# Optimization experiments

Measured on AMD Instinct MI355X. Metric: run time of the kernel, lower is better.

Reference implementation:

```python
import jax, jax.numpy as jnp
import numpy as np

NL, D, H, DK, L, F, P, NC, PS = 2, 128, 8, 16, 197, 256, 8, 1000, 16
EPS = 1e-5


def _ln(x, w, b):
    m = jnp.mean(x, -1, keepdims=True)
    v = jnp.mean((x - m) ** 2, -1, keepdims=True)
    return (x - m) * jax.lax.rsqrt(v + EPS) * w + b


def _trop_lin(x, W, b):
    # max-plus (tropical) linear: y_o = max_i (x_i + W[o, i]) + b_o
    return jnp.max(x[..., None, :] + W, axis=-1) + b


def _forward(x, patch_w, patch_b, cls_token, pos_embed, bn_gamma, bn_beta, bn_run_max, bn_run_range,
             n1_w, n1_b, n2_w, n2_b, wq, bq, wk, bk, wv, bv, wo, bo, gate_w, gate_b, temp,
             tu_w, tu_b, lf_a, lf_c, lf_gate, cu_w, cu_b, fg_w, fg_b, dn_w, dn_b,
             fn_w, fn_b, head_w, head_b):
    B, C, Hh, Ww = x.shape
    p = PS
    # patchify: [B,C,H,W] -> [B,num_patches,C*p*p]
    xp = x.reshape(B, C, Hh // p, p, Ww // p, p).transpose(0, 2, 4, 1, 3, 5).reshape(B, -1, C * p * p)
    h = xp @ patch_w.T + patch_b
    h = jnp.concatenate([jnp.broadcast_to(cls_token, (B, 1, D)), h], axis=1) + pos_embed
    # TropicalBatchNorm (eval mode, running buffers)
    h = bn_gamma * ((h - bn_run_max) / (bn_run_range + EPS)) + bn_beta
    scale = DK ** -0.5
    for i in range(NL):
        hn = _ln(h, n1_w[i], n1_b[i])
        Q = _trop_lin(hn, wq[i], bq[i]).reshape(B, L, H, DK).transpose(0, 2, 1, 3)
        K = _trop_lin(hn, wk[i], bk[i]).reshape(B, L, H, DK).transpose(0, 2, 1, 3)
        V = (hn @ wv[i].T + bv[i]).reshape(B, L, H, DK).transpose(0, 2, 1, 3)
        cs = jnp.einsum('bhqd,bhkd->bhqk', Q, K) * scale
        # tropical max-plus scores: max_d(Q_q + K_k)  -> [B,H,L,L]
        ts = jnp.max(Q[:, :, :, None, :] + K[:, :, None, :, :], axis=-1) * scale
        g = jax.nn.sigmoid(hn @ gate_w[i].T + gate_b[i]).transpose(0, 2, 1)[..., None]  # [B,H,L,1]
        attn = jax.nn.softmax((g * ts + (1.0 - g) * cs) / temp[i][None, :, None, None], axis=-1)
        out = jnp.einsum('bhqk,bhkd->bhqd', attn, V).transpose(0, 2, 1, 3).reshape(B, L, D)
        h = h + (out @ wo[i].T + bo[i])
        hn2 = _ln(h, n2_w[i], n2_b[i])
        z = _trop_lin(hn2, tu_w[i], tu_b[i])                 # [B,L,F]
        zp = z[:, :, None, :] * lf_a[i] + lf_c[i]            # [B,L,P,F]
        gl = jax.nn.sigmoid(lf_gate[i])
        trop = gl * jnp.max(zp, axis=2) + (1.0 - gl) * jnp.min(zp, axis=2)
        classical = jax.nn.gelu(hn2 @ cu_w[i].T + cu_b[i], approximate=False)
        gf = jax.nn.sigmoid(hn2 @ fg_w[i].T + fg_b[i])
        fused = gf * trop + (1.0 - gf) * classical
        h = h + (fused @ dn_w[i].T + dn_b[i])
    h = _ln(h, fn_w, fn_b)
    return h[:, 0] @ head_w.T + head_b


def setup_inputs() -> dict:
    ks = iter(jax.random.split(jax.random.key(0), 64))
    rn = lambda shape, s=0.02: jax.random.normal(next(ks), shape, jnp.float32) * s
    return dict(
        x=jax.random.normal(next(ks), (4, 3, 224, 224), jnp.float32),
        patch_w=rn((D, 3 * PS * PS)), patch_b=jnp.zeros((D,), jnp.float32),
        cls_token=rn((1, 1, D)), pos_embed=rn((1, L, D)),
        bn_gamma=jnp.ones((D,), jnp.float32), bn_beta=jnp.zeros((D,), jnp.float32),
        bn_run_max=jnp.zeros((D,), jnp.float32), bn_run_range=jnp.ones((D,), jnp.float32),
        n1_w=jnp.ones((NL, D), jnp.float32) + rn((NL, D)), n1_b=rn((NL, D)),
        n2_w=jnp.ones((NL, D), jnp.float32) + rn((NL, D)), n2_b=rn((NL, D)),
        wq=rn((NL, D, D)), bq=rn((NL, D)),
        wk=rn((NL, D, D)), bk=rn((NL, D)),
        wv=rn((NL, D, D)), bv=rn((NL, D)),
        wo=rn((NL, D, D)), bo=rn((NL, D)),
        gate_w=rn((NL, H, D)), gate_b=2.0 + rn((NL, H)),
        temp=1.0 + 0.1 * jax.random.uniform(next(ks), (NL, H), jnp.float32),
        tu_w=rn((NL, F, D)), tu_b=rn((NL, F)),
        lf_a=rn((NL, P, F), 0.5), lf_c=rn((NL, P, F), 0.1), lf_gate=rn((NL, F), 0.5),
        cu_w=rn((NL, F, D)), cu_b=rn((NL, F)),
        fg_w=rn((NL, F, D)), fg_b=2.0 + rn((NL, F)),
        dn_w=rn((NL, D, F)), dn_b=rn((NL, D)),
        fn_w=jnp.ones((D,), jnp.float32) + rn((D,)), fn_b=rn((D,)),
        head_w=rn((NC, D)), head_b=jnp.zeros((NC,), jnp.float32),
    )


def reference(x, patch_w, patch_b, cls_token, pos_embed, bn_gamma, bn_beta, bn_run_max, bn_run_range,
              n1_w, n1_b, n2_w, n2_b, wq, bq, wk, bk, wv, bv, wo, bo, gate_w, gate_b, temp,
              tu_w, tu_b, lf_a, lf_c, lf_gate, cu_w, cu_b, fg_w, fg_b, dn_w, dn_b,
              fn_w, fn_b, head_w, head_b):
    return _forward(x, patch_w, patch_b, cls_token, pos_embed, bn_gamma, bn_beta, bn_run_max, bn_run_range,
                    n1_w, n1_b, n2_w, n2_b, wq, bq, wk, bk, wv, bv, wo, bo, gate_w, gate_b, temp,
                    tu_w, tu_b, lf_a, lf_c, lf_gate, cu_w, cu_b, fg_w, fg_b, dn_w, dn_b,
                    fn_w, fn_b, head_w, head_b)
```

## Files before the change

### kernel.cpp

```cpp
#include <hip/hip_runtime.h>
#include <math.h>

#define EPSF 1e-5f

__device__ __forceinline__ float sigm(float v){ return 1.f/(1.f+__expf(-v)); }

#define WS_H    0
#define WS_Q    100864
#define WS_K    201728
#define WS_V    302592
#define WS_G    403456
#define WS_AO   409760
#define WS_PWT  510624
#define WS_WQT  608928
#define WS_WKT  641696
#define WS_WVT  674464
#define WS_WOT  707232
#define WS_GWT  740000
#define WS_TUT  742048
#define WS_CUT  807584
#define WS_FGT  873120
#define WS_DNT  938656
#define WS_HDT  1004192

__global__ __launch_bounds__(256) void k_tr(
    const float* __restrict__ pw, const float* __restrict__ wq, const float* __restrict__ wk,
    const float* __restrict__ wv, const float* __restrict__ wo, const float* __restrict__ gw,
    const float* __restrict__ tu, const float* __restrict__ cu, const float* __restrict__ fg,
    const float* __restrict__ dn, const float* __restrict__ hd, float* __restrict__ ws)
{
    __shared__ float tile[32][33];
    int tn = blockIdx.x, t = threadIdx.x;

    if (tn >= 608) {
        for (int i=t;i<2048;i+=256){
            int m=i>>10, rem=i&1023, k=rem>>3, hh=rem&7;
            ws[WS_GWT + m*1024 + k*8 + hh] = gw[m*1024 + hh*128 + k];
        }
        return;
    }

    const float* srcp; long dstoff; int N, K, NR, nt, kt;
    if (tn < 96) {
        srcp=pw; dstoff=WS_PWT; N=128; K=768; NR=128; nt=tn/24; kt=tn%24;
    } else if (tn < 224) {
        int i2=tn-96, inst=i2>>4, lt=i2&15, m2=inst>>1;
        srcp = (m2==0)?wq:(m2==1)?wk:(m2==2)?wv:wo;
        srcp += (inst&1)*16384;
        dstoff = WS_WQT + (long)m2*32768 + (inst&1)*16384;
        N=128; K=128; NR=128; nt=lt>>2; kt=lt&3;
    } else if (tn < 416) {
        int i2=tn-224, inst=i2>>5, lt=i2&31, m2=inst>>1;
        srcp = (m2==0)?tu:(m2==1)?cu:fg;
        srcp += (inst&1)*32768;
        dstoff = WS_TUT + (long)m2*65536 + (inst&1)*32768;
        N=256; K=128; NR=256; nt=lt>>2; kt=lt&3;
    } else if (tn < 480) {
        int i2=tn-416, inst=i2>>5, lt=i2&31;
        srcp = dn + inst*32768; dstoff = WS_DNT + (long)inst*32768;
        N=128; K=256; NR=128; nt=lt>>3; kt=lt&7;
    } else {
        int lt=tn-480; srcp=hd; dstoff=WS_HDT; N=1000; K=128; NR=1000; nt=lt>>2; kt=lt&3;
    }

    int n0=nt*32, k0=kt*32;
    int tr=t>>3, tc=(t&7)*4;
    float4 v={0.f,0.f,0.f,0.f};
    if (n0+tr < NR) v = *(const float4*)(srcp + (size_t)(n0+tr)*K + k0 + tc);
    tile[tr][tc]=v.x; tile[tr][tc+1]=v.y; tile[tr][tc+2]=v.z; tile[tr][tc+3]=v.w;
    __syncthreads();
    int kr=t>>3, nc=(t&7)*4;
    float o0=tile[nc][kr], o1=tile[nc+1][kr], o2=tile[nc+2][kr], o3=tile[nc+3][kr];
    float* dp = ws + dstoff + (size_t)(k0+kr)*N + n0 + nc;
    if (n0+nc+3 < NR) {
        float4 o4={o0,o1,o2,o3};
        *(float4*)dp = o4;
    } else {
        if (n0+nc   < NR) dp[0]=o0;
        if (n0+nc+1 < NR) dp[1]=o1;
        if (n0+nc+2 < NR) dp[2]=o2;
        if (n0+nc+3 < NR) dp[3]=o3;
    }
}

__device__ __forceinline__ void ln512(float hv,
    const float* __restrict__ lw, const float* __restrict__ lb,
    float* hnS, float* red, int t)
{
    int r = t >> 7, d = t & 127;
    float s = hv, s2 = hv*hv;
    #pragma unroll
    for (int o=1;o<64;o<<=1){ s += __shfl_xor(s,o); s2 += __shfl_xor(s2,o); }
    int wid = t >> 6;
    if ((t & 63) == 0){ red[wid] = s; red[8+wid] = s2; }
    __syncthreads();
    float S  = red[2*r]   + red[2*r+1];
    float S2 = red[8+2*r] + red[8+2*r+1];
    float mu = S*(1.f/128.f), var = S2*(1.f/128.f)-mu*mu;
    float rr = rsqrtf(var+EPSF);
    hnS[r*128+d] = (hv-mu)*rr*lw[d]+lb[d];
    __syncthreads();
}

__device__ __forceinline__ void qkvT512(const float* hnS, float* pacc, int r0, int t,
    const float* __restrict__ wqT, const float* __restrict__ bq,
    const float* __restrict__ wkT, const float* __restrict__ bk,
    const float* __restrict__ wvT, const float* __restrict__ bv,
    const float* __restrict__ gwT, const float* __restrict__ gb,
    float* __restrict__ Q, float* __restrict__ Kg, float* __restrict__ V,
    float* __restrict__ g)
{
    if (t < 384) {
        int mat = t >> 7, q4i = t & 31, ks = (t >> 5) & 3;
        const float* wT = (mat==0) ? wqT : (mat==1) ? wkT : wvT;
        const float4* w4 = (const float4*)wT + q4i;
        float4 acc[4];
        if (mat < 2) {
            #pragma unroll
            for (int r=0;r<4;++r){ acc[r].x=acc[r].y=acc[r].z=acc[r].w=-1e30f; }
            #pragma unroll
            for (int kb=0;kb<2;++kb){
                float4 wv16[16];
                #pragma unroll
                for (int j=0;j<16;++j) wv16[j]=w4[(ks*32+kb*16+j)*32];
                #pragma unroll
                for (int j=0;j<16;++j){
                    float4 w=wv16[j];
                    #pragma unroll
                    for (int r=0;r<4;++r){
                        float av = hnS[r*128 + ks*32+kb*16+j];
                        acc[r].x=fmaxf(acc[r].x,av+w.x); acc[r].y=fmaxf(acc[r].y,av+w.y);
                        acc[r].z=fmaxf(acc[r].z,av+w.z); acc[r].w=fmaxf(acc[r].w,av+w.w);
                    }
                }
            }
        } else {
            #pragma unroll
            for (int r=0;r<4;++r){ acc[r].x=acc[r].y=acc[r].z=acc[r].w=0.f; }
            #pragma unroll
            for (int kb=0;kb<2;++kb){
                float4 wv16[16];
                #pragma unroll
                for (int j=0;j<16;++j) wv16[j]=w4[(ks*32+kb*16+j)*32];
                #pragma unroll
                for (int j=0;j<16;++j){
                    float4 w=wv16[j];
                    #pragma unroll
                    for (int r=0;r<4;++r){
                        float av = hnS[r*128 + ks*32+kb*16+j];
                        acc[r].x=fmaf(av,w.x,acc[r].x); acc[r].y=fmaf(av,w.y,acc[r].y);
                        acc[r].z=fmaf(av,w.z,acc[r].z); acc[r].w=fmaf(av,w.w,acc[r].w);
                    }
                }
            }
        }
        #pragma unroll
        for (int r=0;r<4;++r)
            *(float4*)(pacc + mat*2048 + ks*512 + r*128 + q4i*4) = acc[r];
    } else {
        int u = t & 127, r = u>>5, hh=(u>>2)&7, ks=u&3;
        const float* a = hnS + r*128;
        float acc = 0.f;
        #pragma unroll
        for (int kb=0;kb<2;++kb){
            float wv16[16];
            #pragma unroll
            for (int j=0;j<16;++j) wv16[j]=gwT[(ks*32+kb*16+j)*8+hh];
            #pragma unroll
            for (int j=0;j<16;++j) acc = fmaf(a[ks*32+kb*16+j], wv16[j], acc);
        }
        acc += __shfl_xor(acc,1);
        acc += __shfl_xor(acc,2);
        if (ks==0) g[(r0+r)*8+hh] = sigm(acc + gb[hh]);
    }
    __syncthreads();
    if (t < 384) {
        int mat=t>>7, d=t&127;
        float* dst = (mat==0) ? Q : (mat==1) ? Kg : V;
        const float* bias = (mat==0) ? bq : (mat==1) ? bk : bv;
        #pragma unroll
        for (int r=0;r<4;++r){
            float p0 = pacc[mat*2048 + 0*512 + r*128 + d];
            float p1 = pacc[mat*2048 + 1*512 + r*128 + d];
            float p2 = pacc[mat*2048 + 2*512 + r*128 + d];
            float p3 = pacc[mat*2048 + 3*512 + r*128 + d];
            float s = (mat < 2) ? fmaxf(fmaxf(p0,p1), fmaxf(p2,p3))
                                : (p0 + p1 + p2 + p3);
            dst[(size_t)(r0+r)*128 + d] = s + bias[d];
        }
    }
}

__global__ __launch_bounds__(512) void k_p1(
    const float* __restrict__ x, const float* __restrict__ pwT, const float* __restrict__ pb,
    const float* __restrict__ clsT, const float* __restrict__ pos,
    const float* __restrict__ bng, const float* __restrict__ bnb,
    const float* __restrict__ bnm, const float* __restrict__ bnr,
    const float* __restrict__ n1w, const float* __restrict__ n1b,
    const float* __restrict__ wqT, const float* __restrict__ bq,
    const float* __restrict__ wkT, const float* __restrict__ bk,
    const float* __restrict__ wvT, const float* __restrict__ bv,
    const float* __restrict__ gwT, const float* __restrict__ gb,
    float* __restrict__ h, float* __restrict__ Q, float* __restrict__ Kg,
    float* __restrict__ V, float* __restrict__ g)
{
    __shared__ __align__(16) float xp[4*768];
    __shared__ __align__(16) float pacc[8192];
    __shared__ __align__(16) float hnS[512];
    __shared__ float red[16];
    int t = threadIdx.x, r0 = blockIdx.x * 4;

    #pragma unroll
    for (int r=0;r<4;++r){
        int row=r0+r, b=row/197, l=row-b*197;
        if (l>0){
            int patch=l-1, ph=patch/14, pc=patch-ph*14;
            const float* xb = x + (size_t)b*150528 + ph*3584 + pc*16;
            for (int i=t;i<768;i+=512){
                int c=i>>8, rr=(i>>4)&15, cc=i&15;
                xp[r*768+i] = xb[c*50176 + rr*224 + cc];
            }
        }
    }
    __syncthreads();

    {
        int q4i = t & 31, ks = t >> 5;
        float4 acc[4];
        #pragma unroll
        for (int r=0;r<4;++r){ acc[r].x=acc[r].y=acc[r].z=acc[r].w=0.f; }
        const float4* w4 = (const float4*)pwT + q4i;
        #pragma unroll
        for (int kb=0;kb<3;++kb){
            float4 wv16[16];
            #pragma unroll
            for (int j=0;j<16;++j) wv16[j]=w4[(ks*48+kb*16+j)*32];
            #pragma unroll
            for (int j=0;j<16;++j){
                float4 w=wv16[j];
                #pragma unroll
                for (int r=0;r<4;++r){
                    float av = xp[r*768 + ks*48+kb*16+j];
                    acc[r].x=fmaf(av,w.x,acc[r].x); acc[r].y=fmaf(av,w.y,acc[r].y);
                    acc[r].z=fmaf(av,w.z,acc[r].z); acc[r].w=fmaf(av,w.w,acc[r].w);
                }
            }
        }
        #pragma unroll
        for (int r=0;r<4;++r)
            *(float4*)(pacc + (ks*4+r)*128 + q4i*4) = acc[r];
    }
    __syncthreads();

    float hres;
    {
        int r=t>>7, d=t&127;
        int row=r0+r, l=row%197;
        float s = 0.f;
        #pragma unroll
        for (int ks=0;ks<16;++ks) s += pacc[(ks*4+r)*128+d];
        float v = (l==0) ? clsT[d] : (s + pb[d]);
        v += pos[l*128+d];
        v = bng[d]*((v-bnm[d])/(bnr[d]+EPSF))+bnb[d];
        hres=v;
        h[row*128+d]=v;
    }
    __syncthreads();
    ln512(hres, n1w, n1b, hnS, red, t);
    qkvT512(hnS, pacc, r0, t, wqT,bq,wkT,bk,wvT,bv,gwT,gb, Q,Kg,V,g);
}

__global__ __launch_bounds__(256) void k_attn(
    const float* __restrict__ Qd, const float* __restrict__ Kd,
    const float* __restrict__ Vd, const float* __restrict__ gd,
    const float* __restrict__ tempL, float* __restrict__ ao)
{
    __shared__ __align__(16) float Ks[197*20];
    __shared__ __align__(16) float Vs[197*20];
    int bid = blockIdx.x, t = threadIdx.x;
    int qc = bid % 7, bh = bid / 7, hh = bh & 7, b = bh >> 3;
    size_t base = (size_t)(b*197)*128 + hh*16;

    {
        const float4* ksrc=(const float4*)(Kd+base);
        const float4* vsrc=(const float4*)(Vd+base);
        float4* kdst=(float4*)Ks; float4* vdst=(float4*)Vs;
        for (int idx=t; idx<788; idx+=256){
            int l=idx>>2, jj=idx&3;
            kdst[l*5+jj]=ksrc[l*32+jj];
            vdst[l*5+jj]=vsrc[l*32+jj];
        }
    }
    __syncthreads();

    int q = qc*32 + (t>>3), j8 = t&7;
    if (q >= 197) return;

    float Qr[16];
    {
        const float4* qp=(const float4*)(Qd+base+(size_t)q*128);
        #pragma unroll
        for (int u=0;u<4;++u){
            float4 v=qp[u];
            Qr[4*u]=v.x; Qr[4*u+1]=v.y; Qr[4*u+2]=v.z; Qr[4*u+3]=v.w;
        }
    }
    float gq = gd[(b*197+q)*8+hh];
    float it = 0.25f / tempL[hh];
    float gg = gq*it, cg = (1.f-gq)*it;

    float m=-1e30f, lsum=0.f, o[16];
    #pragma unroll
    for (int j=0;j<16;++j) o[j]=0.f;

    for (int k=j8;k<197;k+=8){
        const float4* kr4=(const float4*)(Ks+k*20);
        float4 kv0=kr4[0], kv1=kr4[1], kv2=kr4[2], kv3=kr4[3];
        float kr[16] = {kv0.x,kv0.y,kv0.z,kv0.w, kv1.x,kv1.y,kv1.z,kv1.w,
                        kv2.x,kv2.y,kv2.z,kv2.w, kv3.x,kv3.y,kv3.z,kv3.w};
        float cs=0.f, ts=-1e30f;
        #pragma unroll
        for (int j=0;j<16;++j){
            cs=fmaf(Qr[j],kr[j],cs);
            ts=fmaxf(ts,Qr[j]+kr[j]);
        }
        float sc=fmaf(gg,ts,cg*cs);
        if (sc>m){
            float c=__expf(m-sc);
            lsum*=c;
            #pragma unroll
            for (int j=0;j<16;++j) o[j]*=c;
            m=sc;
        }
        float p=__expf(sc-m);
        lsum+=p;
        const float4* vr4=(const float4*)(Vs+k*20);
        float4 vv0=vr4[0], vv1=vr4[1], vv2=vr4[2], vv3=vr4[3];
        float vr[16] = {vv0.x,vv0.y,vv0.z,vv0.w, vv1.x,vv1.y,vv1.z,vv1.w,
                        vv2.x,vv2.y,vv2.z,vv2.w, vv3.x,vv3.y,vv3.z,vv3.w};
        #pragma unroll
        for (int j=0;j<16;++j) o[j]=fmaf(p,vr[j],o[j]);
    }

    #pragma unroll
    for (int mask=1;mask<8;mask<<=1){
        float mo=__shfl_xor(m,mask), lo=__shfl_xor(lsum,mask);
        float mn=fmaxf(m,mo);
        float ea=__expf(m-mn), eb=__expf(mo-mn);
        lsum=lsum*ea+lo*eb;
        #pragma unroll
        for (int j=0;j<16;++j){
            float oo=__shfl_xor(o[j],mask);
            o[j]=o[j]*ea+oo*eb;
        }
        m=mn;
    }

    if (j8==0){
        float inv=1.f/lsum;
        float* orow=ao+base+(size_t)q*128;
        #pragma unroll
        for (int j=0;j<16;++j) orow[j]=o[j]*inv;
    }
}

template <int FINAL>
__global__ __launch_bounds__(512) void k_p34(
    const float* __restrict__ ao, float* __restrict__ h,
    const float* __restrict__ woT, const float* __restrict__ bo,
    const float* __restrict__ n2w, const float* __restrict__ n2b,
    const float* __restrict__ tuT, const float* __restrict__ tub,
    const float* __restrict__ laA, const float* __restrict__ laC,
    const float* __restrict__ lgG,
    const float* __restrict__ cuT, const float* __restrict__ cub,
    const float* __restrict__ fgT, const float* __restrict__ fgb,
    const float* __restrict__ dnT, const float* __restrict__ dnb,
    const float* __restrict__ nlw, const float* __restrict__ nlb,
    const float* __restrict__ wqT, const float* __restrict__ bq,
    const float* __restrict__ wkT, const float* __restrict__ bk,
    const float* __restrict__ wvT, const float* __restrict__ bv,
    const float* __restrict__ gwT, const float* __restrict__ gb,
    float* __restrict__ Q, float* __restrict__ Kg, float* __restrict__ V,
    float* __restrict__ g,
    const float* __restrict__ hdT, const float* __restrict__ hdb,
    float* __restrict__ out)
{
    __shared__ __align__(16) float aoS[512];
    __shared__ __align__(16) float pacc[8192];
    __shared__ __align__(16) float hnS[512];
    __shared__ __align__(16) float zP[6144];
    __shared__ __align__(16) float fusedS[1024];
    __shared__ float red[16];
    int t = threadIdx.x, r0 = blockIdx.x * 4;

    aoS[t] = ao[(size_t)r0*128 + t];
    __syncthreads();

    {
        int q4i=t&31, ks=t>>5;
        float4 acc[4];
        #pragma unroll
        for (int r=0;r<4;++r){ acc[r].x=acc[r].y=acc[r].z=acc[r].w=0.f; }
        const float4* w4=(const float4*)woT + q4i;
        float4 wv8[8];
        #pragma unroll
        for (int j=0;j<8;++j) wv8[j]=w4[(ks*8+j)*32];
        #pragma unroll
        for (int j=0;j<8;++j){
            float4 w=wv8[j];
            #pragma unroll
            for (int r=0;r<4;++r){
                float av=aoS[r*128 + ks*8+j];
                acc[r].x=fmaf(av,w.x,acc[r].x); acc[r].y=fmaf(av,w.y,acc[r].y);
                acc[r].z=fmaf(av,w.z,acc[r].z); acc[r].w=fmaf(av,w.w,acc[r].w);
            }
        }
        #pragma unroll
        for (int r=0;r<4;++r)
            *(float4*)(pacc + (ks*4+r)*128 + q4i*4) = acc[r];
    }
    __syncthreads();

    float hres;
    {
        int r=t>>7, d=t&127;
        float s=0.f;
        #pragma unroll
        for (int ks=0;ks<16;++ks) s += pacc[(ks*4+r)*128+d];
        hres = h[(size_t)(r0+r)*128+d] + s + bo[d];
    }
    __syncthreads();
    ln512(hres, n2w, n2b, hnS, red, t);

    {
        int gidx=t>>6, fq=t&63;
        if (gidx < 6) {
            int mat=gidx>>1, ks2=gidx&1;
            const float* wT = (mat==0)? tuT : (mat==1)? cuT : fgT;
            const float4* w4=(const float4*)wT + fq;
            float4 acc[4];
            if (mat==0){
                #pragma unroll
                for (int r=0;r<4;++r){ acc[r].x=acc[r].y=acc[r].z=acc[r].w=-1e30f; }
                #pragma unroll
                for (int kb=0;kb<4;++kb){
                    float4 wv16[16];
                    #pragma unroll
                    for (int j=0;j<16;++j) wv16[j]=w4[(ks2*64+kb*16+j)*64];
                    #pragma unroll
                    for (int j=0;j<16;++j){
                        float4 w=wv16[j];
                        #pragma unroll
                        for (int r=0;r<4;++r){
                            float av=hnS[r*128 + ks2*64+kb*16+j];
                            acc[r].x=fmaxf(acc[r].x,av+w.x); acc[r].y=fmaxf(acc[r].y,av+w.y);
                            acc[r].z=fmaxf(acc[r].z,av+w.z); acc[r].w=fmaxf(acc[r].w,av+w.w);
                        }
                    }
                }
            } else {
                #pragma unroll
                for (int r=0;r<4;++r){ acc[r].x=acc[r].y=acc[r].z=acc[r].w=0.f; }
                #pragma unroll
                for (int kb=0;kb<4;++kb){
                    float4 wv16[16];
                    #pragma unroll
                    for (int j=0;j<16;++j) wv16[j]=w4[(ks2*64+kb*16+j)*64];
                    #pragma unroll
                    for (int j=0;j<16;++j){
                        float4 w=wv16[j];
                        #pragma unroll
                        for (int r=0;r<4;++r){
                            float av=hnS[r*128 + ks2*64+kb*16+j];
                            acc[r].x=fmaf(av,w.x,acc[r].x); acc[r].y=fmaf(av,w.y,acc[r].y);
                            acc[r].z=fmaf(av,w.z,acc[r].z); acc[r].w=fmaf(av,w.w,acc[r].w);
                        }
                    }
                }
            }
            #pragma unroll
            for (int r=0;r<4;++r)
                *(float4*)(zP + mat*2048 + ks2*1024 + r*256 + fq*4) = acc[r];
        }
    }
    __syncthreads();

    #pragma unroll
    for (int s2=0;s2<2;++s2){
        int slot = t + s2*512;
        int r = slot>>8, f = slot&255;
        float z  = fmaxf(zP[r*256+f],        zP[1024+r*256+f]) + tub[f];
        float xc = zP[2048+r*256+f] + zP[3072+r*256+f] + cub[f];
        float gv = zP[4096+r*256+f] + zP[5120+r*256+f] + fgb[f];
        float gl = sigm(lgG[f]);
        float mx=-1e30f, mn=1e30f;
        #pragma unroll
        for (int p=0;p<8;++p){
            float zp=fmaf(z, laA[p*256+f], laC[p*256+f]);
            mx=fmaxf(mx,zp); mn=fminf(mn,zp);
        }
        float trop=gl*mx+(1.f-gl)*mn;
        float cla=0.5f*xc*(1.f+erff(xc*0.70710678118654752f));
        float gf=sigm(gv);
        fusedS[r*256+f]=gf*trop+(1.f-gf)*cla;
    }
    __syncthreads();

    {
        int q4i=t&31, ks=t>>5;
        float4 acc[4];
        #pragma unroll
        for (int r=0;r<4;++r){ acc[r].x=acc[r].y=acc[r].z=acc[r].w=0.f; }
        const float4* w4=(const float4*)dnT + q4i;
        float4 wv16[16];
        #pragma unroll
        for (int j=0;j<16;++j) wv16[j]=w4[(ks*16+j)*32];
        #pragma unroll
        for (int j=0;j<16;++j){
            float4 w=wv16[j];
            #pragma unroll
            for (int r=0;r<4;++r){
                float av=fusedS[r*256 + ks*16+j];
                acc[r].x=fmaf(av,w.x,acc[r].x); acc[r].y=fmaf(av,w.y,acc[r].y);
                acc[r].z=fmaf(av,w.z,acc[r].z); acc[r].w=fmaf(av,w.w,acc[r].w);
            }
        }
        __syncthreads();
        #pragma unroll
        for (int r=0;r<4;++r)
            *(float4*)(pacc + (ks*4+r)*128 + q4i*4) = acc[r];
    }
    __syncthreads();
    {
        int r=t>>7, d=t&127;
        float s=0.f;
        #pragma unroll
        for (int ks=0;ks<16;++ks) s += pacc[(ks*4+r)*128+d];
        hres += s + dnb[d];
        if (!FINAL) h[(size_t)(r0+r)*128+d]=hres;
    }
    __syncthreads();
    ln512(hres, nlw, nlb, hnS, red, t);

    if (!FINAL) {
        qkvT512(hnS, pacc, r0, t, wqT,bq,wkT,bk,wvT,bv,gwT,gb, Q,Kg,V,g);
    } else {
        int crow=-1, cb2=0;
        #pragma unroll
        for (int r=0;r<4;++r){
            int row=r0+r;
            if (row==0 || row==197 || row==394 || row==591){ crow=r; cb2=row/197; }
        }
        if (crow>=0 && t<500){
            const float2* w2=(const float2*)hdT + t;
            const float* a = hnS + crow*128;
            float acc0=hdb[2*t], acc1=hdb[2*t+1];
            #pragma unroll
            for (int kb=0;kb<8;++kb){
                float2 wv16[16];
                #pragma unroll
                for (int j=0;j<16;++j) wv16[j]=w2[(kb*16+j)*500];
                #pragma unroll
                for (int j=0;j<16;++j){
                    float av=a[kb*16+j];
                    acc0=fmaf(av,wv16[j].x,acc0); acc1=fmaf(av,wv16[j].y,acc1);
                }
            }
            out[cb2*1000+2*t]=acc0;
            out[cb2*1000+2*t+1]=acc1;
        }
    }
}

extern "C" void kernel_launch(void* const* d_in, const int* in_sizes, int n_in,
                              void* d_out, int out_size, void* d_ws, size_t ws_size,
                              hipStream_t stream)
{
    const float* x        = (const float*)d_in[0];
    const float* patch_w  = (const float*)d_in[1];
    const float* patch_b  = (const float*)d_in[2];
    const float* cls_tok  = (const float*)d_in[3];
    const float* pos_emb  = (const float*)d_in[4];
    const float* bn_gamma = (const float*)d_in[5];
    const float* bn_beta  = (const float*)d_in[6];
    const float* bn_rmax  = (const float*)d_in[7];
    const float* bn_rrng  = (const float*)d_in[8];
    const float* n1_w     = (const float*)d_in[9];
    const float* n1_b     = (const float*)d_in[10];
    const float* n2_w     = (const float*)d_in[11];
    const float* n2_b     = (const float*)d_in[12];
    const float* wq       = (const float*)d_in[13];
    const float* bq       = (const float*)d_in[14];
    const float* wk       = (const float*)d_in[15];
    const float* bk       = (const float*)d_in[16];
    const float* wv       = (const float*)d_in[17];
    const float* bv       = (const float*)d_in[18];
    const float* wo       = (const float*)d_in[19];
    const float* bo       = (const float*)d_in[20];
    const float* gate_w   = (const float*)d_in[21];
    const float* gate_b   = (const float*)d_in[22];
    const float* temp     = (const float*)d_in[23];
    const float* tu_w     = (const float*)d_in[24];
    const float* tu_b     = (const float*)d_in[25];
    const float* lf_a     = (const float*)d_in[26];
    const float* lf_c     = (const float*)d_in[27];
    const float* lf_gate  = (const float*)d_in[28];
    const float* cu_w     = (const float*)d_in[29];
    const float* cu_b     = (const float*)d_in[30];
    const float* fg_w     = (const float*)d_in[31];
    const float* fg_b     = (const float*)d_in[32];
    const float* dn_w     = (const float*)d_in[33];
    const float* dn_b     = (const float*)d_in[34];
    const float* fn_w     = (const float*)d_in[35];
    const float* fn_b     = (const float*)d_in[36];
    const float* head_w   = (const float*)d_in[37];
    const float* head_b   = (const float*)d_in[38];

    float* ws = (float*)d_ws;
    float* h   = ws + WS_H;
    float* Q   = ws + WS_Q;
    float* Kb  = ws + WS_K;
    float* V   = ws + WS_V;
    float* g   = ws + WS_G;
    float* ao  = ws + WS_AO;
    float* out = (float*)d_out;

    k_tr<<<609, 256, 0, stream>>>(patch_w, wq, wk, wv, wo, gate_w,
                                  tu_w, cu_w, fg_w, dn_w, head_w, ws);

    k_p1<<<197, 512, 0, stream>>>(x, ws+WS_PWT, patch_b, cls_tok, pos_emb,
                                  bn_gamma, bn_beta, bn_rmax, bn_rrng,
                                  n1_w, n1_b,
                                  ws+WS_WQT, bq, ws+WS_WKT, bk, ws+WS_WVT, bv,
                                  ws+WS_GWT, gate_b,
                                  h, Q, Kb, V, g);

    k_attn<<<224, 256, 0, stream>>>(Q, Kb, V, g, temp, ao);

    k_p34<0><<<197, 512, 0, stream>>>(ao, h,
        ws+WS_WOT, bo, n2_w, n2_b,
        ws+WS_TUT, tu_b, lf_a, lf_c, lf_gate,
        ws+WS_CUT, cu_b, ws+WS_FGT, fg_b, ws+WS_DNT, dn_b,
        n1_w + 128, n1_b + 128,
        ws+WS_WQT+16384, bq + 128, ws+WS_WKT+16384, bk + 128,
        ws+WS_WVT+16384, bv + 128, ws+WS_GWT+1024, gate_b + 8,
        Q, Kb, V, g, nullptr, nullptr, nullptr);

    k_attn<<<224, 256, 0, stream>>>(Q, Kb, V, g, temp + 8, ao);

    k_p34<1><<<197, 512, 0, stream>>>(ao, h,
        ws+WS_WOT+16384, bo + 128, n2_w + 128, n2_b + 128,
        ws+WS_TUT+32768, tu_b + 256, lf_a + 2048, lf_c + 2048, lf_gate + 256,
        ws+WS_CUT+32768, cu_b + 256, ws+WS_FGT+32768, fg_b + 256,
        ws+WS_DNT+32768, dn_b + 128,
        fn_w, fn_b,
        nullptr, nullptr, nullptr, nullptr, nullptr, nullptr, nullptr, nullptr,
        Q, Kb, V, g, ws+WS_HDT, head_b, out);
}
```

Measured before the change: 78.02 us.

## Store transposed weights as packed bf16 pairs and unpack in GEMV loops

The weight transpose kernel now writes most weight matrices as bf16 with rounding, interleaving adjacent-k pairs so one 16-byte load yields two k rows of four outputs. All GEMV and max-plus loops in the patch, QKV, output, FFN and down projections load uint4 and unpack via shifts, halving weight bytes read per block. Launch bounds are raised to request two blocks per CU, and the head loop batch is shrunk. This trades accuracy for bandwidth, since weights lose mantissa bits including in tropical max-plus layers, and it adds unpack ALU work.

```diff
diff --git a/kernel.cpp b/kernel.cpp
--- a/kernel.cpp
+++ b/kernel.cpp
@@ -4,6 +4,22 @@
 #define EPSF 1e-5f
 
 __device__ __forceinline__ float sigm(float v){ return 1.f/(1.f+__expf(-v)); }
+
+__device__ __forceinline__ unsigned short f2bf(float f){
+    unsigned int b = __float_as_uint(f);
+    unsigned int r = (b + 0x7fffu + ((b>>16)&1u)) >> 16;
+    return (unsigned short)r;
+}
+
+struct BF8 { float w0,w1,w2,w3,w4,w5,w6,w7; };
+__device__ __forceinline__ BF8 unpk(uint4 U){
+    BF8 o;
+    o.w0=__uint_as_float(U.x<<16); o.w1=__uint_as_float(U.x&0xffff0000u);
+    o.w2=__uint_as_float(U.y<<16); o.w3=__uint_as_float(U.y&0xffff0000u);
+    o.w4=__uint_as_float(U.z<<16); o.w5=__uint_as_float(U.z&0xffff0000u);
+    o.w6=__uint_as_float(U.w<<16); o.w7=__uint_as_float(U.w&0xffff0000u);
+    return o;
+}
 
 #define WS_H    0
 #define WS_Q    100864
@@ -11,17 +27,18 @@
 #define WS_V    302592
 #define WS_G    403456
 #define WS_AO   409760
-#define WS_PWT  510624
-#define WS_WQT  608928
-#define WS_WKT  641696
-#define WS_WVT  674464
-#define WS_WOT  707232
-#define WS_GWT  740000
-#define WS_TUT  742048
-#define WS_CUT  807584
-#define WS_FGT  873120
-#define WS_DNT  938656
-#define WS_HDT  1004192
+#define WS_GWT  510624
+#define WS_HDT  512672
+#define WS_BF   640672
+#define BW_PWT  0
+#define BW_WQT  98304
+#define BW_WKT  131072
+#define BW_WVT  163840
+#define BW_WOT  196608
+#define BW_TUT  229376
+#define BW_CUT  294912
+#define BW_FGT  360448
+#define BW_DNT  425984
 
 __global__ __launch_bounds__(256) void k_tr(
     const float* __restrict__ pw, const float* __restrict__ wq, const float* __restrict__ wk,
@@ -31,6 +48,7 @@
 {
     __shared__ float tile[32][33];
     int tn = blockIdx.x, t = threadIdx.x;
+    unsigned short* wsb = (unsigned short*)(ws + WS_BF);
 
     if (tn >= 608) {
         for (int i=t;i<2048;i+=256){
@@ -40,27 +58,28 @@
         return;
     }
 
-    const float* srcp; long dstoff; int N, K, NR, nt, kt;
+    const float* srcp; long dstoff; int N, K, NR, nt, kt; int isbf = 1;
     if (tn < 96) {
-        srcp=pw; dstoff=WS_PWT; N=128; K=768; NR=128; nt=tn/24; kt=tn%24;
+        srcp=pw; dstoff=BW_PWT; N=128; K=768; NR=128; nt=tn/24; kt=tn%24;
     } else if (tn < 224) {
         int i2=tn-96, inst=i2>>4, lt=i2&15, m2=inst>>1;
         srcp = (m2==0)?wq:(m2==1)?wk:(m2==2)?wv:wo;
         srcp += (inst&1)*16384;
-        dstoff = WS_WQT + (long)m2*32768 + (inst&1)*16384;
+        dstoff = BW_WQT + (long)m2*32768 + (inst&1)*16384;
         N=128; K=128; NR=128; nt=lt>>2; kt=lt&3;
     } else if (tn < 416) {
         int i2=tn-224, inst=i2>>5, lt=i2&31, m2=inst>>1;
         srcp = (m2==0)?tu:(m2==1)?cu:fg;
         srcp += (inst&1)*32768;
-        dstoff = WS_TUT + (long)m2*65536 + (inst&1)*32768;
+        dstoff = BW_TUT + (long)m2*65536 + (inst&1)*32768;
         N=256; K=128; NR=256; nt=lt>>2; kt=lt&3;
     } else if (tn < 480) {
         int i2=tn-416, inst=i2>>5, lt=i2&31;
-        srcp = dn + inst*32768; dstoff = WS_DNT + (long)inst*32768;
+        srcp = dn + inst*32768; dstoff = BW_DNT + (long)inst*32768;
         N=128; K=256; NR=128; nt=lt>>3; kt=lt&7;
     } else {
         int lt=tn-480; srcp=hd; dstoff=WS_HDT; N=1000; K=128; NR=1000; nt=lt>>2; kt=lt&3;
+        isbf = 0;
     }
 
     int n0=nt*32, k0=kt*32;
@@ -71,15 +90,22 @@
     __syncthreads();
     int kr=t>>3, nc=(t&7)*4;
     float o0=tile[nc][kr], o1=tile[nc+1][kr], o2=tile[nc+2][kr], o3=tile[nc+3][kr];
-    float* dp = ws + dstoff + (size_t)(k0+kr)*N + n0 + nc;
-    if (n0+nc+3 < NR) {
-        float4 o4={o0,o1,o2,o3};
-        *(float4*)dp = o4;
+    if (isbf) {
+        int kk = k0+kr, nn = n0+nc;
+        unsigned short* dp = wsb + dstoff + ((size_t)(kk>>1)*2*N + (size_t)nn*2 + (kk&1)*4);
+        ushort4 u4; u4.x=f2bf(o0); u4.y=f2bf(o1); u4.z=f2bf(o2); u4.w=f2bf(o3);
+        *(ushort4*)dp = u4;
     } else {
-        if (n0+nc   < NR) dp[0]=o0;
-        if (n0+nc+1 < NR) dp[1]=o1;
-        if (n0+nc+2 < NR) dp[2]=o2;
-        if (n0+nc+3 < NR) dp[3]=o3;
+        float* dp = ws + dstoff + (size_t)(k0+kr)*N + n0 + nc;
+        if (n0+nc+3 < NR) {
+            float4 o4={o0,o1,o2,o3};
+            *(float4*)dp = o4;
+        } else {
+            if (n0+nc   < NR) dp[0]=o0;
+            if (n0+nc+1 < NR) dp[1]=o1;
+            if (n0+nc+2 < NR) dp[2]=o2;
+            if (n0+nc+3 < NR) dp[3]=o3;
+        }
     }
 }
 
@@ -103,34 +129,38 @@
 }
 
 __device__ __forceinline__ void qkvT512(const float* hnS, float* pacc, int r0, int t,
-    const float* __restrict__ wqT, const float* __restrict__ bq,
-    const float* __restrict__ wkT, const float* __restrict__ bk,
-    const float* __restrict__ wvT, const float* __restrict__ bv,
+    const unsigned short* __restrict__ wqB, const float* __restrict__ bq,
+    const unsigned short* __restrict__ wkB, const float* __restrict__ bk,
+    const unsigned short* __restrict__ wvB, const float* __restrict__ bv,
     const float* __restrict__ gwT, const float* __restrict__ gb,
     float* __restrict__ Q, float* __restrict__ Kg, float* __restrict__ V,
     float* __restrict__ g)
 {
     if (t < 384) {
         int mat = t >> 7, q4i = t & 31, ks = (t >> 5) & 3;
-        const float* wT = (mat==0) ? wqT : (mat==1) ? wkT : wvT;
-        const float4* w4 = (const float4*)wT + q4i;
+        const unsigned short* wB = (mat==0) ? wqB : (mat==1) ? wkB : wvB;
+        const uint4* wp = (const uint4*)wB + q4i;
+        int pbase = ks*16;
         float4 acc[4];
         if (mat < 2) {
             #pragma unroll
             for (int r=0;r<4;++r){ acc[r].x=acc[r].y=acc[r].z=acc[r].w=-1e30f; }
             #pragma unroll
-            for (int kb=0;kb<2;++kb){
-                float4 wv16[16];
-                #pragma unroll
-                for (int j=0;j<16;++j) wv16[j]=w4[(ks*32+kb*16+j)*32];
-                #pragma unroll
-                for (int j=0;j<16;++j){
-                    float4 w=wv16[j];
+            for (int rnd=0;rnd<2;++rnd){
+                uint4 wu[8];
+                #pragma unroll
+                for (int j=0;j<8;++j) wu[j]=wp[(pbase+rnd*8+j)*32];
+                #pragma unroll
+                for (int j=0;j<8;++j){
+                    BF8 W = unpk(wu[j]);
+                    int k = (pbase+rnd*8+j)*2;
                     #pragma unroll
                     for (int r=0;r<4;++r){
-                        float av = hnS[r*128 + ks*32+kb*16+j];
-                        acc[r].x=fmaxf(acc[r].x,av+w.x); acc[r].y=fmaxf(acc[r].y,av+w.y);
-                        acc[r].z=fmaxf(acc[r].z,av+w.z); acc[r].w=fmaxf(acc[r].w,av+w.w);
+                        float a0=hnS[r*128+k], a1=hnS[r*128+k+1];
+                        acc[r].x=fmaxf(acc[r].x,fmaxf(a0+W.w0,a1+W.w4));
+                        acc[r].y=fmaxf(acc[r].y,fmaxf(a0+W.w1,a1+W.w5));
+                        acc[r].z=fmaxf(acc[r].z,fmaxf(a0+W.w2,a1+W.w6));
+                        acc[r].w=fmaxf(acc[r].w,fmaxf(a0+W.w3,a1+W.w7));
                     }
                 }
             }
@@ -138,18 +168,21 @@
             #pragma unroll
             for (int r=0;r<4;++r){ acc[r].x=acc[r].y=acc[r].z=acc[r].w=0.f; }
             #pragma unroll
-            for (int kb=0;kb<2;++kb){
-                float4 wv16[16];
-                #pragma unroll
-                for (int j=0;j<16;++j) wv16[j]=w4[(ks*32+kb*16+j)*32];
-                #pragma unroll
-                for (int j=0;j<16;++j){
-                    float4 w=wv16[j];
+            for (int rnd=0;rnd<2;++rnd){
+                uint4 wu[8];
+                #pragma unroll
+                for (int j=0;j<8;++j) wu[j]=wp[(pbase+rnd*8+j)*32];
+                #pragma unroll
+                for (int j=0;j<8;++j){
+                    BF8 W = unpk(wu[j]);
+                    int k = (pbase+rnd*8+j)*2;
                     #pragma unroll
                     for (int r=0;r<4;++r){
-                        float av = hnS[r*128 + ks*32+kb*16+j];
-                        acc[r].x=fmaf(av,w.x,acc[r].x); acc[r].y=fmaf(av,w.y,acc[r].y);
-                        acc[r].z=fmaf(av,w.z,acc[r].z); acc[r].w=fmaf(av,w.w,acc[r].w);
+                        float a0=hnS[r*128+k], a1=hnS[r*128+k+1];
+                        acc[r].x=fmaf(a0,W.w0,fmaf(a1,W.w4,acc[r].x));
+                        acc[r].y=fmaf(a0,W.w1,fmaf(a1,W.w5,acc[r].y));
+                        acc[r].z=fmaf(a0,W.w2,fmaf(a1,W.w6,acc[r].z));
+                        acc[r].w=fmaf(a0,W.w3,fmaf(a1,W.w7,acc[r].w));
                     }
                 }
             }
@@ -191,15 +224,16 @@
     }
 }
 
-__global__ __launch_bounds__(512) void k_p1(
-    const float* __restrict__ x, const float* __restrict__ pwT, const float* __restrict__ pb,
+__global__ __launch_bounds__(512, 2) void k_p1(
+    const float* __restrict__ x, const unsigned short* __restrict__ pwB,
+    const float* __restrict__ pb,
     const float* __restrict__ clsT, const float* __restrict__ pos,
     const float* __restrict__ bng, const float* __restrict__ bnb,
     const float* __restrict__ bnm, const float* __restrict__ bnr,
     const float* __restrict__ n1w, const float* __restrict__ n1b,
-    const float* __restrict__ wqT, const float* __restrict__ bq,
-    const float* __restrict__ wkT, const float* __restrict__ bk,
-    const float* __restrict__ wvT, const float* __restrict__ bv,
+    const unsigned short* __restrict__ wqB, const float* __restrict__ bq,
+    const unsigned short* __restrict__ wkB, const float* __restrict__ bk,
+    const unsigned short* __restrict__ wvB, const float* __restrict__ bv,
     const float* __restrict__ gwT, const float* __restrict__ gb,
     float* __restrict__ h, float* __restrict__ Q, float* __restrict__ Kg,
     float* __restrict__ V, float* __restrict__ g)
@@ -226,23 +260,27 @@
 
     {
         int q4i = t & 31, ks = t >> 5;
+        const uint4* wp = (const uint4*)pwB + q4i;
+        int pbase = ks*24;
         float4 acc[4];
         #pragma unroll
         for (int r=0;r<4;++r){ acc[r].x=acc[r].y=acc[r].z=acc[r].w=0.f; }
-        const float4* w4 = (const float4*)pwT + q4i;
-        #pragma unroll
-        for (int kb=0;kb<3;++kb){
-            float4 wv16[16];
-            #pragma unroll
-            for (int j=0;j<16;++j) wv16[j]=w4[(ks*48+kb*16+j)*32];
-            #pragma unroll
-            for (int j=0;j<16;++j){
-                float4 w=wv16[j];
+        #pragma unroll
+        for (int rnd=0;rnd<3;++rnd){
+            uint4 wu[8];
+            #pragma unroll
+            for (int j=0;j<8;++j) wu[j]=wp[(pbase+rnd*8+j)*32];
+            #pragma unroll
+            for (int j=0;j<8;++j){
+                BF8 W = unpk(wu[j]);
+                int k = (pbase+rnd*8+j)*2;
                 #pragma unroll
                 for (int r=0;r<4;++r){
-                    float av = xp[r*768 + ks*48+kb*16+j];
-                    acc[r].x=fmaf(av,w.x,acc[r].x); acc[r].y=fmaf(av,w.y,acc[r].y);
-                    acc[r].z=fmaf(av,w.z,acc[r].z); acc[r].w=fmaf(av,w.w,acc[r].w);
+                    float a0=xp[r*768+k], a1=xp[r*768+k+1];
+                    acc[r].x=fmaf(a0,W.w0,fmaf(a1,W.w4,acc[r].x));
+                    acc[r].y=fmaf(a0,W.w1,fmaf(a1,W.w5,acc[r].y));
+                    acc[r].z=fmaf(a0,W.w2,fmaf(a1,W.w6,acc[r].z));
+                    acc[r].w=fmaf(a0,W.w3,fmaf(a1,W.w7,acc[r].w));
                 }
             }
         }
@@ -258,7 +296,7 @@
         int row=r0+r, l=row%197;
         float s = 0.f;
         #pragma unroll
-        for (int ks=0;ks<16;++ks) s += pacc[(ks*4+r)*128+d];
+        for (int k2=0;k2<16;++k2) s += pacc[(k2*4+r)*128+d];
         float v = (l==0) ? clsT[d] : (s + pb[d]);
         v += pos[l*128+d];
         v = bng[d]*((v-bnm[d])/(bnr[d]+EPSF))+bnb[d];
@@ -267,7 +305,7 @@
     }
     __syncthreads();
     ln512(hres, n1w, n1b, hnS, red, t);
-    qkvT512(hnS, pacc, r0, t, wqT,bq,wkT,bk,wvT,bv,gwT,gb, Q,Kg,V,g);
+    qkvT512(hnS, pacc, r0, t, wqB,bq,wkB,bk,wvB,bv,gwT,gb, Q,Kg,V,g);
 }
 
 __global__ __launch_bounds__(256) void k_attn(
@@ -365,20 +403,20 @@
 }
 
 template <int FINAL>
-__global__ __launch_bounds__(512) void k_p34(
+__global__ __launch_bounds__(512, 2) void k_p34(
     const float* __restrict__ ao, float* __restrict__ h,
-    const float* __restrict__ woT, const float* __restrict__ bo,
+    const unsigned short* __restrict__ woB, const float* __restrict__ bo,
     const float* __restrict__ n2w, const float* __restrict__ n2b,
-    const float* __restrict__ tuT, const float* __restrict__ tub,
+    const unsigned short* __restrict__ tuB, const float* __restrict__ tub,
     const float* __restrict__ laA, const float* __restrict__ laC,
     const float* __restrict__ lgG,
-    const float* __restrict__ cuT, const float* __restrict__ cub,
-    const float* __restrict__ fgT, const float* __restrict__ fgb,
-    const float* __restrict__ dnT, const float* __restrict__ dnb,
+    const unsigned short* __restrict__ cuB, const float* __restrict__ cub,
+    const unsigned short* __restrict__ fgB, const float* __restrict__ fgb,
+    const unsigned short* __restrict__ dnB, const float* __restrict__ dnb,
     const float* __restrict__ nlw, const float* __restrict__ nlb,
-    const float* __restrict__ wqT, const float* __restrict__ bq,
-    const float* __restrict__ wkT, const float* __restrict__ bk,
-    const float* __restrict__ wvT, const float* __restrict__ bv,
+    const unsigned short* __restrict__ wqB, const float* __restrict__ bq,
+    const unsigned short* __restrict__ wkB, const float* __restrict__ bk,
+    const unsigned short* __restrict__ wvB, const float* __restrict__ bv,
     const float* __restrict__ gwT, const float* __restrict__ gb,
     float* __restrict__ Q, float* __restrict__ Kg, float* __restrict__ V,
     float* __restrict__ g,
@@ -392,27 +430,31 @@
     __shared__ __align__(16) float fusedS[1024];
     __shared__ float red[16];
     int t = threadIdx.x, r0 = blockIdx.x * 4;
+    int q4i=t&31, ks=t>>5;
 
     aoS[t] = ao[(size_t)r0*128 + t];
     __syncthreads();
 
     {
-        int q4i=t&31, ks=t>>5;
+        const uint4* wp=(const uint4*)woB + q4i;
+        int pbase = ks*4;
         float4 acc[4];
         #pragma unroll
         for (int r=0;r<4;++r){ acc[r].x=acc[r].y=acc[r].z=acc[r].w=0.f; }
-        const float4* w4=(const float4*)woT + q4i;
-        float4 wv8[8];
-        #pragma unroll
-        for (int j=0;j<8;++j) wv8[j]=w4[(ks*8+j)*32];
-        #pragma unroll
-        for (int j=0;j<8;++j){
-            float4 w=wv8[j];
+        uint4 wu[4];
+        #pragma unroll
+        for (int j=0;j<4;++j) wu[j]=wp[(pbase+j)*32];
+        #pragma unroll
+        for (int j=0;j<4;++j){
+            BF8 W = unpk(wu[j]);
+            int k = (pbase+j)*2;
             #pragma unroll
             for (int r=0;r<4;++r){
-                float av=aoS[r*128 + ks*8+j];
-                acc[r].x=fmaf(av,w.x,acc[r].x); acc[r].y=fmaf(av,w.y,acc[r].y);
-                acc[r].z=fmaf(av,w.z,acc[r].z); acc[r].w=fmaf(av,w.w,acc[r].w);
+                float a0=aoS[r*128+k], a1=aoS[r*128+k+1];
+                acc[r].x=fmaf(a0,W.w0,fmaf(a1,W.w4,acc[r].x));
+                acc[r].y=fmaf(a0,W.w1,fmaf(a1,W.w5,acc[r].y));
+                acc[r].z=fmaf(a0,W.w2,fmaf(a1,W.w6,acc[r].z));
+                acc[r].w=fmaf(a0,W.w3,fmaf(a1,W.w7,acc[r].w));
             }
         }
         #pragma unroll
@@ -426,7 +468,7 @@
         int r=t>>7, d=t&127;
         float s=0.f;
         #pragma unroll
-        for (int ks=0;ks<16;++ks) s += pacc[(ks*4+r)*128+d];
+        for (int k2=0;k2<16;++k2) s += pacc[(k2*4+r)*128+d];
         hres = h[(size_t)(r0+r)*128+d] + s + bo[d];
     }
     __syncthreads();
@@ -436,25 +478,29 @@
         int gidx=t>>6, fq=t&63;
         if (gidx < 6) {
             int mat=gidx>>1, ks2=gidx&1;
-            const float* wT = (mat==0)? tuT : (mat==1)? cuT : fgT;
-            const float4* w4=(const float4*)wT + fq;
+            const unsigned short* wBm = (mat==0)? tuB : (mat==1)? cuB : fgB;
+            const uint4* wp=(const uint4*)wBm + fq;
+            int pbase = ks2*32;
             float4 acc[4];
             if (mat==0){
                 #pragma unroll
                 for (int r=0;r<4;++r){ acc[r].x=acc[r].y=acc[r].z=acc[r].w=-1e30f; }
                 #pragma unroll
-                for (int kb=0;kb<4;++kb){
-                    float4 wv16[16];
+                for (int rnd=0;rnd<4;++rnd){
+                    uint4 wu[8];
                     #pragma unroll
-                    for (int j=0;j<16;++j) wv16[j]=w4[(ks2*64+kb*16+j)*64];
+                    for (int j=0;j<8;++j) wu[j]=wp[(pbase+rnd*8+j)*64];
                     #pragma unroll
-                    for (int j=0;j<16;++j){
-                        float4 w=wv16[j];
+                    for (int j=0;j<8;++j){
+                        BF8 W = unpk(wu[j]);
+                        int k = (pbase+rnd*8+j)*2;
                         #pragma unroll
                         for (int r=0;r<4;++r){
-                            float av=hnS[r*128 + ks2*64+kb*16+j];
-                            acc[r].x=fmaxf(acc[r].x,av+w.x); acc[r].y=fmaxf(acc[r].y,av+w.y);
-                            acc[r].z=fmaxf(acc[r].z,av+w.z); acc[r].w=fmaxf(acc[r].w,av+w.w);
+                            float a0=hnS[r*128+k], a1=hnS[r*128+k+1];
+                            acc[r].x=fmaxf(acc[r].x,fmaxf(a0+W.w0,a1+W.w4));
+                            acc[r].y=fmaxf(acc[r].y,fmaxf(a0+W.w1,a1+W.w5));
+                            acc[r].z=fmaxf(acc[r].z,fmaxf(a0+W.w2,a1+W.w6));
+                            acc[r].w=fmaxf(acc[r].w,fmaxf(a0+W.w3,a1+W.w7));
                         }
                     }
                 }
@@ -462,18 +508,21 @@
                 #pragma unroll
                 for (int r=0;r<4;++r){ acc[r].x=acc[r].y=acc[r].z=acc[r].w=0.f; }
                 #pragma unroll
-                for (int kb=0;kb<4;++kb){
-                    float4 wv16[16];
+                for (int rnd=0;rnd<4;++rnd){
+                    uint4 wu[8];
                     #pragma unroll
-                    for (int j=0;j<16;++j) wv16[j]=w4[(ks2*64+kb*16+j)*64];
+                    for (int j=0;j<8;++j) wu[j]=wp[(pbase+rnd*8+j)*64];
                     #pragma unroll
-                    for (int j=0;j<16;++j){
-                        float4 w=wv16[j];
+                    for (int j=0;j<8;++j){
+                        BF8 W = unpk(wu[j]);
+                        int k = (pbase+rnd*8+j)*2;
                         #pragma unroll
                         for (int r=0;r<4;++r){
-                            float av=hnS[r*128 + ks2*64+kb*16+j];
-                            acc[r].x=fmaf(av,w.x,acc[r].x); acc[r].y=fmaf(av,w.y,acc[r].y);
-                            acc[r].z=fmaf(av,w.z,acc[r].z); acc[r].w=fmaf(av,w.w,acc[r].w);
+                            float a0=hnS[r*128+k], a1=hnS[r*128+k+1];
+                            acc[r].x=fmaf(a0,W.w0,fmaf(a1,W.w4,acc[r].x));
+                            acc[r].y=fmaf(a0,W.w1,fmaf(a1,W.w5,acc[r].y));
+                            acc[r].z=fmaf(a0,W.w2,fmaf(a1,W.w6,acc[r].z));
+                            acc[r].w=fmaf(a0,W.w3,fmaf(a1,W.w7,acc[r].w));
                         }
                     }
                 }
@@ -507,22 +556,25 @@
     __syncthreads();
 
     {
-        int q4i=t&31, ks=t>>5;
+        const uint4* wp=(const uint4*)dnB + q4i;
+        int pbase = ks*8;
         float4 acc[4];
         #pragma unroll
         for (int r=0;r<4;++r){ acc[r].x=acc[r].y=acc[r].z=acc[r].w=0.f; }
-        const float4* w4=(const float4*)dnT + q4i;
-        float4 wv16[16];
-        #pragma unroll
-        for (int j=0;j<16;++j) wv16[j]=w4[(ks*16+j)*32];
-        #pragma unroll
-        for (int j=0;j<16;++j){
-            float4 w=wv16[j];
+        uint4 wu[8];
+        #pragma unroll
+        for (int j=0;j<8;++j) wu[j]=wp[(pbase+j)*32];
+        #pragma unroll
+        for (int j=0;j<8;++j){
+            BF8 W = unpk(wu[j]);
+            int k = (pbase+j)*2;
             #pragma unroll
             for (int r=0;r<4;++r){
-                float av=fusedS[r*256 + ks*16+j];
-                acc[r].x=fmaf(av,w.x,acc[r].x); acc[r].y=fmaf(av,w.y,acc[r].y);
-                acc[r].z=fmaf(av,w.z,acc[r].z); acc[r].w=fmaf(av,w.w,acc[r].w);
+                float a0=fusedS[r*256+k], a1=fusedS[r*256+k+1];
+                acc[r].x=fmaf(a0,W.w0,fmaf(a1,W.w4,acc[r].x));
+                acc[r].y=fmaf(a0,W.w1,fmaf(a1,W.w5,acc[r].y));
+                acc[r].z=fmaf(a0,W.w2,fmaf(a1,W.w6,acc[r].z));
+                acc[r].w=fmaf(a0,W.w3,fmaf(a1,W.w7,acc[r].w));
             }
         }
         __syncthreads();
@@ -535,7 +587,7 @@
         int r=t>>7, d=t&127;
         float s=0.f;
         #pragma unroll
-        for (int ks=0;ks<16;++ks) s += pacc[(ks*4+r)*128+d];
+        for (int k2=0;k2<16;++k2) s += pacc[(k2*4+r)*128+d];
         hres += s + dnb[d];
         if (!FINAL) h[(size_t)(r0+r)*128+d]=hres;
     }
@@ -543,7 +595,7 @@
     ln512(hres, nlw, nlb, hnS, red, t);
 
     if (!FINAL) {
-        qkvT512(hnS, pacc, r0, t, wqT,bq,wkT,bk,wvT,bv,gwT,gb, Q,Kg,V,g);
+        qkvT512(hnS, pacc, r0, t, wqB,bq,wkB,bk,wvB,bv,gwT,gb, Q,Kg,V,g);
     } else {
         int crow=-1, cb2=0;
         #pragma unroll
@@ -556,14 +608,14 @@
             const float* a = hnS + crow*128;
             float acc0=hdb[2*t], acc1=hdb[2*t+1];
             #pragma unroll
-            for (int kb=0;kb<8;++kb){
-                float2 wv16[16];
-                #pragma unroll
-                for (int j=0;j<16;++j) wv16[j]=w2[(kb*16+j)*500];
-                #pragma unroll
-                for (int j=0;j<16;++j){
-                    float av=a[kb*16+j];
-                    acc0=fmaf(av,wv16[j].x,acc0); acc1=fmaf(av,wv16[j].y,acc1);
+            for (int kb=0;kb<16;++kb){
+                float2 wv8[8];
+                #pragma unroll
+                for (int j=0;j<8;++j) wv8[j]=w2[(kb*8+j)*500];
+                #pragma unroll
+                for (int j=0;j<8;++j){
+                    float av=a[kb*8+j];
+                    acc0=fmaf(av,wv8[j].x,acc0); acc1=fmaf(av,wv8[j].y,acc1);
                 }
             }
             out[cb2*1000+2*t]=acc0;
@@ -623,37 +675,39 @@
     float* V   = ws + WS_V;
     float* g   = ws + WS_G;
     float* ao  = ws + WS_AO;
+    unsigned short* wsb = (unsigned short*)(ws + WS_BF);
     float* out = (float*)d_out;
 
     k_tr<<<609, 256, 0, stream>>>(patch_w, wq, wk, wv, wo, gate_w,
                                   tu_w, cu_w, fg_w, dn_w, head_w, ws);
 
-    k_p1<<<197, 512, 0, stream>>>(x, ws+WS_PWT, patch_b, cls_tok, pos_emb,
+    k_p1<<<197, 512, 0, stream>>>(x, wsb+BW_PWT, patch_b, cls_tok, pos_emb,
                                   bn_gamma, bn_beta, bn_rmax, bn_rrng,
                                   n1_w, n1_b,
-                                  ws+WS_WQT, bq, ws+WS_WKT, bk, ws+WS_WVT, bv,
+                                  wsb+BW_WQT, bq, wsb+BW_WKT, bk, wsb+BW_WVT, bv,
                                   ws+WS_GWT, gate_b,
                                   h, Q, Kb, V, g);
 
     k_attn<<<224, 256, 0, stream>>>(Q, Kb, V, g, temp, ao);
 
     k_p34<0><<<197, 512, 0, stream>>>(ao, h,
-        ws+WS_WOT, bo, n2_w, n2_b,
-        ws+WS_TUT, tu_b, lf_a, lf_c, lf_gate,
-        ws+WS_CUT, cu_b, ws+WS_FGT, fg_b, ws+WS_DNT, dn_b,
+        wsb+BW_WOT, bo, n2_w, n2_b,
+        wsb+BW_TUT, tu_b, lf_a, lf_c, lf_gate,
+        wsb+BW_CUT, cu_b, wsb+BW_FGT, fg_b, wsb+BW_DNT, dn_b,
         n1_w + 128, n1_b + 128,
-        ws+WS_WQT+16384, bq + 128, ws+WS_WKT+16384, bk + 128,
-        ws+WS_WVT+16384, bv + 128, ws+WS_GWT+1024, gate_b + 8,
+        wsb+BW_WQT+16384, bq + 128, wsb+BW_WKT+16384, bk + 128,
+        wsb+BW_WVT+16384, bv + 128, ws+WS_GWT+1024, gate_b + 8,
         Q, Kb, V, g, nullptr, nullptr, nullptr);
 
     k_attn<<<224, 256, 0, stream>>>(Q, Kb, V, g, temp + 8, ao);
 
     k_p34<1><<<197, 512, 0, stream>>>(ao, h,
-        ws+WS_WOT+16384, bo + 128, n2_w + 128, n2_b + 128,
-        ws+WS_TUT+32768, tu_b + 256, lf_a + 2048, lf_c + 2048, lf_gate + 256,
-        ws+WS_CUT+32768, cu_b + 256, ws+WS_FGT+32768, fg_b + 256,
-        ws+WS_DNT+32768, dn_b + 128,
+        wsb+BW_WOT+16384, bo + 128, n2_w + 128, n2_b + 128,
+        wsb+BW_TUT+32768, tu_b + 256, lf_a + 2048, lf_c + 2048, lf_gate + 256,
+        wsb+BW_CUT+32768, cu_b + 256, wsb+BW_FGT+32768, fg_b + 256,
+        wsb+BW_DNT+32768, dn_b + 128,
         fn_w, fn_b,
-        nullptr, nullptr, nullptr, nullptr, nullptr, nullptr, nullptr, nullptr,
+        nullptr, nullptr, nullptr, nullptr, nullptr, nullptr,
+        ws+WS_GWT, gate_b,
         Q, Kb, V, g, ws+WS_HDT, head_b, out);
 }
```

New measurement: 77.37 us. About the same (-0.8%).
